# Kernel tuning notes

Measured on AMD Instinct MI355X. Metric: run time of the kernel, lower is better.

## Reference

```python
import jax, jax.numpy as jnp
import numpy as np

# --- configuration constants (from OpticalDotProductConfiguration) ---
INPUT_BITS = 8
ADC_BITS = 8
DAC_VMIN, DAC_VMAX = 0.0, 1.0
ADC_VMAX = 1.0
OPT_GAIN = 10.0
AWG_XTALK = 0.01
MZM_VMIN, MZM_VMAX = 0.0, 1.0
MZM_LOSS = 10.0 ** (-0.5 / 10.0)   # loss_dB_to_linear(0.5)
YB_LOSS = 10.0 ** (-0.3 / 10.0)
MRR_LOSS = 10.0 ** (-0.5 / 10.0)
MRR_XTALK = 0.01
PD_RESP = 1.0
PD_DARK = 1e-12
PD_R = 50.0
PD_HZ = 10.0 * 1e9
PD_T = 300.0
TIA_GAIN = 100.0
K_B = 1.380649e-23
Q_E = 1.602176634e-19

B, N = 4096, 8192


def conv_same(x, kernel):
    # x: [B, N], kernel: [K]; torch F.conv1d = cross-correlation, same as lax conv
    out = jax.lax.conv_general_dilated(
        x[:, None, :], kernel[None, None, :], (1,), 'SAME')
    return out[:, 0, :]


def setup_inputs() -> dict:
    key = jax.random.key(0)
    ks = jax.random.split(key, 6)
    return {
        'x': jax.random.normal(ks[0], (B, N), dtype=jnp.float32),
        'weights': jax.random.normal(ks[1], (N,), dtype=jnp.float32),
        'noise_tp': jax.random.normal(ks[2], (B,), dtype=jnp.float32),
        'noise_sp': jax.random.normal(ks[3], (B,), dtype=jnp.float32),
        'noise_tn': jax.random.normal(ks[4], (B,), dtype=jnp.float32),
        'noise_sn': jax.random.normal(ks[5], (B,), dtype=jnp.float32),
    }


def reference(x, weights, noise_tp, noise_sp, noise_tn, noise_sn):
    dt = x.dtype
    # software_implemented_transformation
    wnorm = jnp.max(jnp.abs(weights))
    wnorm = jnp.where(wnorm <= 1e-9, jnp.asarray(1.0, dt), wnorm)
    wt = weights / wnorm
    w_abs = jnp.abs(wt)            # weight DAC is identity for weights
    w_pos = wt >= 0                # [N] bool

    t_pos = x > 0                  # [B, N]
    ax = jnp.abs(x)
    inorm = jnp.max(ax, axis=1)
    inorm = jnp.where(inorm <= 1e-9, jnp.asarray(1.0, dt), inorm)[:, None]
    maxq_in = 2 ** INPUT_BITS - 1
    q = jnp.round(ax / inorm * maxq_in)

    # input DAC
    d = jnp.round(jnp.clip(q, 0.0, maxq_in)) / maxq_in
    d = DAC_VMIN + (DAC_VMAX - DAC_VMIN) * d

    # laser: gain + AWG crosstalk conv
    lk = jnp.array([AWG_XTALK / 4, AWG_XTALK, 1.0, AWG_XTALK, AWG_XTALK / 4], dtype=dt)
    l = conv_same(d * OPT_GAIN, lk)

    # MZM
    m = l * w_abs / (MZM_VMAX - MZM_VMIN) * (YB_LOSS * MZM_LOSS)

    # MRR: masked split, crosstalk conv, loss, reduce over N
    pm = jnp.logical_not(jnp.logical_xor(w_pos[None, :], t_pos)).astype(dt)
    mk = jnp.array([MRR_XTALK / 4, MRR_XTALK, 1.0, MRR_XTALK, MRR_XTALK / 4], dtype=dt)
    pos_sum = jnp.sum(conv_same(m * pm, mk) * MRR_LOSS, axis=1)        # [B]
    neg_sum = jnp.sum(conv_same(m * (1.0 - pm), mk) * MRR_LOSS, axis=1)

    # photodiode with injected noise
    thermal_c = 4.0 * K_B * PD_T * PD_HZ / PD_R
    shot_c = 2.0 * Q_E * PD_HZ

    def pd(t, nth, nsh):
        t = t * PD_RESP + PD_DARK
        t = t + nth * thermal_c
        return t * (1.0 + nsh * shot_c)

    cur = pd(pos_sum, noise_tp, noise_sp) - pd(neg_sum, noise_tn, noise_sn)

    # TIA
    v = jnp.abs(cur * TIA_GAIN)
    sign = (cur >= 0).astype(dt) * 2.0 - 1.0

    # ADC
    sf = (2 ** ADC_BITS - 1) / ADC_VMAX
    va = jnp.round(jnp.clip(v, 0.0, ADC_VMAX) * sf) / sf
    out = va * sign

    scale = wnorm / (2.0 ** (ADC_BITS - INPUT_BITS))
    scale = scale / (OPT_GAIN * TIA_GAIN * MRR_LOSS * YB_LOSS * MZM_LOSS)
    scale = scale / ((PD_RESP + PD_RESP) / 2.0)
    out = out * (scale * inorm[:, 0])
    return out
```

## Files before the change

### kernel.cpp

```cpp
#include <hip/hip_runtime.h>
#include <math.h>

#define NCOL 8192
#define BT   512
#define EPT  16

#define MZM_LOSS_D 0.8912509381337456
#define YB_LOSS_D  0.9332543007969910
#define MRR_LOSS_D 0.8912509381337456

__global__ __launch_bounds__(BT, 6)
void odp_main(const float* __restrict__ x, const float* __restrict__ w,
              const float* __restrict__ ntp, const float* __restrict__ nsp,
              const float* __restrict__ ntn, const float* __restrict__ nsn,
              float* __restrict__ out)
{
    __shared__ float  redX[8];
    __shared__ float  redW[8];
    __shared__ float  redT[8];
    __shared__ double redD[8];
    __shared__ double corrd[4];

    const int t    = threadIdx.x;
    const int lane = t & 63;
    const int wid  = t >> 6;
    const int b    = blockIdx.x;

    const float v_ntp = ntp[b], v_nsp = nsp[b], v_ntn = ntn[b], v_nsn = nsn[b];

    const float*  __restrict__ xrow = x + (size_t)b * NCOL;
    const float4* __restrict__ xr4  = (const float4*)xrow;
    const float4* __restrict__ w4   = (const float4*)w;

    float xf[EPT];
    const int hL = (t > 0)      ? (t * EPT - 2)   : 0;
    const int hR = (t < BT - 1) ? (t * EPT + EPT) : (NCOL - 2);
    const float2 hxL = *(const float2*)(xrow + hL);
    const float2 hxR = *(const float2*)(xrow + hR);

    float mx = 0.f;
#pragma unroll
    for (int j = 0; j < 4; ++j) {
        const float4 xv = xr4[t * 4 + j];
        xf[4*j+0]=xv.x; xf[4*j+1]=xv.y; xf[4*j+2]=xv.z; xf[4*j+3]=xv.w;
        mx = fmaxf(mx, fmaxf(fmaxf(fabsf(xv.x), fabsf(xv.y)),
                             fmaxf(fabsf(xv.z), fabsf(xv.w))));
    }
#pragma unroll
    for (int off = 32; off; off >>= 1)
        mx = fmaxf(mx, __shfl_down(mx, off));
    if (lane == 0) redX[wid] = mx;
    __syncthreads();

    float inorm = redX[0];
#pragma unroll
    for (int i = 1; i < 8; ++i) inorm = fmaxf(inorm, redX[i]);
    inorm = (inorm <= 1e-9f) ? 1.f : inorm;

    const double inv_d = 1.0 / (double)inorm;
    const float  y     = (float)inv_d;

    float wf[EPT];
    float mw = 0.f;
#pragma unroll
    for (int j = 0; j < 4; ++j) {
        const float4 wv = w4[t * 4 + j];
        wf[4*j+0]=wv.x; wf[4*j+1]=wv.y; wf[4*j+2]=wv.z; wf[4*j+3]=wv.w;
        mw = fmaxf(mw, fmaxf(fmaxf(fabsf(wv.x), fabsf(wv.y)),
                             fmaxf(fabsf(wv.z), fabsf(wv.w))));
    }

    float Q[EPT + 4];
#pragma unroll
    for (int c = 0; c < EPT; ++c) {
        const float a  = fabsf(xf[c]);
        const float q0 = a * y;
        const float r  = fmaf(-inorm, q0, a);
        Q[c + 2] = rintf(fmaf(r, y, q0) * 255.f);
    }
    {
        const float aL0 = fabsf(hxL.x), aL1 = fabsf(hxL.y);
        const float aR0 = fabsf(hxR.x), aR1 = fabsf(hxR.y);
        float q0, r;
        q0 = aL0 * y; r = fmaf(-inorm, q0, aL0); Q[0]  = rintf(fmaf(r, y, q0) * 255.f);
        q0 = aL1 * y; r = fmaf(-inorm, q0, aL1); Q[1]  = rintf(fmaf(r, y, q0) * 255.f);
        q0 = aR0 * y; r = fmaf(-inorm, q0, aR0); Q[18] = rintf(fmaf(r, y, q0) * 255.f);
        q0 = aR1 * y; r = fmaf(-inorm, q0, aR1); Q[19] = rintf(fmaf(r, y, q0) * 255.f);
        if (t == 0)      { Q[0]  = 0.f; Q[1]  = 0.f; }
        if (t == BT - 1) { Q[18] = 0.f; Q[19] = 0.f; }
    }

    float Dv[4] = {0.f,0.f,0.f,0.f}, Tv[4] = {0.f,0.f,0.f,0.f};
    double cD = 0.0, cT = 0.0;
    const double DE0 = -((double)0.01f + (double)0.0025f);
    const double DE1 = -((double)0.0025f);

#pragma unroll
    for (int c = 0; c < EPT; ++c) {
        const float s1 = Q[c + 1] + Q[c + 3];
        const float s2 = Q[c]     + Q[c + 4];
        float conv = fmaf(0.01f, s1, Q[c + 2]);
        conv = fmaf(0.0025f, s2, conv);
        const float sel = (xf[c] > 0.f) ? wf[c] : -wf[c];
        Dv[c & 3] = fmaf(conv, sel,        Dv[c & 3]);
        Tv[c & 3] = fmaf(conv, fabsf(sel), Tv[c & 3]);
    }
    if (t == 0) {
#pragma unroll
        for (int c = 0; c < 2; ++c) {
            const float s1 = Q[c + 1] + Q[c + 3];
            const float s2 = Q[c]     + Q[c + 4];
            float conv = fmaf(0.01f, s1, Q[c + 2]);
            conv = fmaf(0.0025f, s2, conv);
            const float sel = (xf[c] > 0.f) ? wf[c] : -wf[c];
            const double de = (c == 0) ? DE0 : DE1;
            cD += de * (double)(conv * sel);
            cT += de * (double)(conv * fabsf(sel));
        }
    }
    if (t == BT - 1) {
#pragma unroll
        for (int c = EPT - 2; c < EPT; ++c) {
            const float s1 = Q[c + 1] + Q[c + 3];
            const float s2 = Q[c]     + Q[c + 4];
            float conv = fmaf(0.01f, s1, Q[c + 2]);
            conv = fmaf(0.0025f, s2, conv);
            const float sel = (xf[c] > 0.f) ? wf[c] : -wf[c];
            const double de = (c == EPT - 1) ? DE0 : DE1;
            cD += de * (double)(conv * sel);
            cT += de * (double)(conv * fabsf(sel));
        }
    }

    double accD = ((double)Dv[0] + (double)Dv[1]) + ((double)Dv[2] + (double)Dv[3]);
    float  accT = (Tv[0] + Tv[1]) + (Tv[2] + Tv[3]);

#pragma unroll
    for (int off = 32; off; off >>= 1) {
        accD += __shfl_down(accD, off);
        accT += __shfl_down(accT, off);
        mw    = fmaxf(mw, __shfl_down(mw, off));
    }
    if (lane == 0)   { redD[wid] = accD; redT[wid] = accT; redW[wid] = mw; }
    if (t == 0)      { corrd[0] = cD; corrd[1] = cT; }
    if (t == BT - 1) { corrd[2] = cD; corrd[3] = cT; }
    __syncthreads();

    if (t == 0) {
        double D = 0.0, T = 0.0;
        float wnorm = redW[0];
#pragma unroll
        for (int i = 0; i < 8; ++i) {
            D += redD[i]; T += (double)redT[i];
            wnorm = fmaxf(wnorm, redW[i]);
        }
        wnorm = (wnorm <= 1e-9f) ? 1.f : wnorm;

        const double E_MID = 1.0 + 2.0 * (double)0.01f + 2.0 * (double)0.0025f;
        D = D * E_MID + (corrd[0] + corrd[2]);
        T = T * E_MID + (corrd[1] + corrd[3]);

        const double Kd = (10.0 / 255.0) * (YB_LOSS_D * MZM_LOSS_D) / (double)wnorm;
        const double ps = (T + D) * 0.5 * Kd * MRR_LOSS_D;
        const double ns = (T - D) * 0.5 * Kd * MRR_LOSS_D;

        const float thermal_f = 3.3135576e-12f;
        const float shot_f    = 3.204353268e-9f;

        double tp_ = ps + 1e-12 + (double)(v_ntp * thermal_f);
        tp_ *= (double)(1.0f + v_nsp * shot_f);
        double tn_ = ns + 1e-12 + (double)(v_ntn * thermal_f);
        tn_ *= (double)(1.0f + v_nsn * shot_f);

        const double cur = tp_ - tn_;
        double v = fabs(cur * 100.0);
        v = fmin(v, 1.0);
        const double va  = rint(v * 255.0) * (1.0 / 255.0);
        const double sgn = (cur >= 0.0) ? 1.0 : -1.0;
        const double scale = (double)wnorm /
            (10.0 * 100.0 * MRR_LOSS_D * YB_LOSS_D * MZM_LOSS_D);
        out[b] = (float)(va * sgn * scale * (double)inorm);
    }
}

extern "C" void kernel_launch(void* const* d_in, const int* in_sizes, int n_in,
                              void* d_out, int out_size, void* d_ws, size_t ws_size,
                              hipStream_t stream) {
    const float* x   = (const float*)d_in[0];
    const float* w   = (const float*)d_in[1];
    const float* ntp = (const float*)d_in[2];
    const float* nsp = (const float*)d_in[3];
    const float* ntn = (const float*)d_in[4];
    const float* nsn = (const float*)d_in[5];
    float* out = (float*)d_out;
    odp_main<<<dim3(out_size), dim3(BT), 0, stream>>>(x, w, ntp, nsp, ntn, nsn, out);
}
```

Baseline: 32.67 us.

## Process eight rows per block with double-buffered async global-to-LDS loads

```diff
diff --git a/kernel.cpp b/kernel.cpp
--- a/kernel.cpp
+++ b/kernel.cpp
@@ -4,62 +4,51 @@
 #define NCOL 8192
 #define BT   512
 #define EPT  16
+#define ROWS 8
+#define NF4  2048
 
 #define MZM_LOSS_D 0.8912509381337456
 #define YB_LOSS_D  0.9332543007969910
 #define MRR_LOSS_D 0.8912509381337456
 
-__global__ __launch_bounds__(BT, 6)
+typedef __attribute__((address_space(3))) void       lds_void_t;
+typedef const __attribute__((address_space(1))) void g_void_t;
+
+static __device__ __forceinline__ void lds_barrier() {
+    asm volatile("s_waitcnt lgkmcnt(0)" ::: "memory");
+    __builtin_amdgcn_s_barrier();
+}
+
+static __device__ __forceinline__ int swz(int g) { return g ^ ((g >> 3) & 7); }
+
+#define QF(dst, a_) do {                                   \
+    const float a__  = (a_);                               \
+    const float q0__ = a__ * y;                            \
+    const float r__  = fmaf(-inorm, q0__, a__);            \
+    (dst) = rintf(fmaf(r__, y, q0__) * 255.f);             \
+} while (0)
+
+__global__ __launch_bounds__(BT, 4)
 void odp_main(const float* __restrict__ x, const float* __restrict__ w,
               const float* __restrict__ ntp, const float* __restrict__ nsp,
               const float* __restrict__ ntn, const float* __restrict__ nsn,
               float* __restrict__ out)
 {
-    __shared__ float  redX[8];
-    __shared__ float  redW[8];
-    __shared__ float  redT[8];
+    __shared__ float4 xs[2][NF4];
+    __shared__ float  redX[8], redW[8], redT[8];
     __shared__ double redD[8];
     __shared__ double corrd[4];
 
     const int t    = threadIdx.x;
     const int lane = t & 63;
     const int wid  = t >> 6;
-    const int b    = blockIdx.x;
-
-    const float v_ntp = ntp[b], v_nsp = nsp[b], v_ntn = ntn[b], v_nsn = nsn[b];
-
-    const float*  __restrict__ xrow = x + (size_t)b * NCOL;
-    const float4* __restrict__ xr4  = (const float4*)xrow;
-    const float4* __restrict__ w4   = (const float4*)w;
-
-    float xf[EPT];
-    const int hL = (t > 0)      ? (t * EPT - 2)   : 0;
-    const int hR = (t < BT - 1) ? (t * EPT + EPT) : (NCOL - 2);
-    const float2 hxL = *(const float2*)(xrow + hL);
-    const float2 hxR = *(const float2*)(xrow + hR);
-
-    float mx = 0.f;
-#pragma unroll
-    for (int j = 0; j < 4; ++j) {
-        const float4 xv = xr4[t * 4 + j];
-        xf[4*j+0]=xv.x; xf[4*j+1]=xv.y; xf[4*j+2]=xv.z; xf[4*j+3]=xv.w;
-        mx = fmaxf(mx, fmaxf(fmaxf(fabsf(xv.x), fabsf(xv.y)),
-                             fmaxf(fabsf(xv.z), fabsf(xv.w))));
-    }
-#pragma unroll
-    for (int off = 32; off; off >>= 1)
-        mx = fmaxf(mx, __shfl_down(mx, off));
-    if (lane == 0) redX[wid] = mx;
-    __syncthreads();
-
-    float inorm = redX[0];
-#pragma unroll
-    for (int i = 1; i < 8; ++i) inorm = fmaxf(inorm, redX[i]);
-    inorm = (inorm <= 1e-9f) ? 1.f : inorm;
-
-    const double inv_d = 1.0 / (double)inorm;
-    const float  y     = (float)inv_d;
-
+    const int r0   = blockIdx.x * ROWS;
+
+    const double DE0 = -((double)0.01f + (double)0.0025f);
+    const double DE1 = -((double)0.0025f);
+    const double E_MID = 1.0 + 2.0 * (double)0.01f + 2.0 * (double)0.0025f;
+
+    const float4* __restrict__ w4 = (const float4*)w;
     float wf[EPT];
     float mw = 0.f;
 #pragma unroll
@@ -70,117 +59,168 @@
                              fmaxf(fabsf(wv.z), fabsf(wv.w))));
     }
 
-    float Q[EPT + 4];
-#pragma unroll
-    for (int c = 0; c < EPT; ++c) {
-        const float a  = fabsf(xf[c]);
-        const float q0 = a * y;
-        const float r  = fmaf(-inorm, q0, a);
-        Q[c + 2] = rintf(fmaf(r, y, q0) * 255.f);
-    }
-    {
-        const float aL0 = fabsf(hxL.x), aL1 = fabsf(hxL.y);
-        const float aR0 = fabsf(hxR.x), aR1 = fabsf(hxR.y);
-        float q0, r;
-        q0 = aL0 * y; r = fmaf(-inorm, q0, aL0); Q[0]  = rintf(fmaf(r, y, q0) * 255.f);
-        q0 = aL1 * y; r = fmaf(-inorm, q0, aL1); Q[1]  = rintf(fmaf(r, y, q0) * 255.f);
-        q0 = aR0 * y; r = fmaf(-inorm, q0, aR0); Q[18] = rintf(fmaf(r, y, q0) * 255.f);
-        q0 = aR1 * y; r = fmaf(-inorm, q0, aR1); Q[19] = rintf(fmaf(r, y, q0) * 255.f);
+#define STAGE(BUF, ROW) do {                                                  \
+    const float* xr_ = x + (size_t)(ROW) * NCOL;                              \
+    _Pragma("unroll")                                                         \
+    for (int k = 0; k < 4; ++k) {                                             \
+        const int phys_ = ((wid * 4 + k) << 6) | lane;                        \
+        __builtin_amdgcn_global_load_lds(                                     \
+            (g_void_t*)(xr_ + 4 * swz(phys_)),                                \
+            (lds_void_t*)&xs[BUF][(wid * 4 + k) << 6], 16, 0, 0);             \
+    }                                                                         \
+} while (0)
+
+    STAGE(0, r0);
+
+    int wi[4];
+#pragma unroll
+    for (int k = 0; k < 4; ++k) wi[k] = swz(4 * t + k);
+    const int hiL = swz((t > 0)      ? (4 * t - 1) : 0);
+    const int hiR = swz((t < BT - 1) ? (4 * t + 4) : (NF4 - 1));
+
+    float wnorm = 1.f;
+    float ov[ROWS];
+
+#pragma unroll
+    for (int r = 0; r < ROWS; ++r) {
+        const int buf = r & 1;
+        if (r < ROWS - 1) {
+            STAGE(buf ^ 1, r0 + r + 1);
+            asm volatile("s_waitcnt vmcnt(4)" ::: "memory");
+        } else {
+            asm volatile("s_waitcnt vmcnt(0)" ::: "memory");
+        }
+
+        float xf[EPT];
+#pragma unroll
+        for (int k = 0; k < 4; ++k) {
+            const float4 v = xs[buf][wi[k]];
+            xf[4*k+0]=v.x; xf[4*k+1]=v.y; xf[4*k+2]=v.z; xf[4*k+3]=v.w;
+        }
+        float mx = 0.f;
+#pragma unroll
+        for (int c = 0; c < EPT; ++c) mx = fmaxf(mx, fabsf(xf[c]));
+#pragma unroll
+        for (int off = 32; off; off >>= 1)
+            mx = fmaxf(mx, __shfl_down(mx, off));
+        if (lane == 0) redX[wid] = mx;
+        lds_barrier();
+
+        float inorm = redX[0];
+#pragma unroll
+        for (int i = 1; i < 8; ++i) inorm = fmaxf(inorm, redX[i]);
+        inorm = (inorm <= 1e-9f) ? 1.f : inorm;
+        const double inv_d = 1.0 / (double)inorm;
+        const float  y     = (float)inv_d;
+
+        const float4 hv1 = xs[buf][hiL];
+        const float4 hv2 = xs[buf][hiR];
+
+        float Q[EPT + 4];
+#pragma unroll
+        for (int c = 0; c < EPT; ++c) QF(Q[c + 2], fabsf(xf[c]));
+        QF(Q[0],  fabsf(hv1.z)); QF(Q[1],  fabsf(hv1.w));
+        QF(Q[18], fabsf(hv2.x)); QF(Q[19], fabsf(hv2.y));
         if (t == 0)      { Q[0]  = 0.f; Q[1]  = 0.f; }
         if (t == BT - 1) { Q[18] = 0.f; Q[19] = 0.f; }
-    }
-
-    float Dv[4] = {0.f,0.f,0.f,0.f}, Tv[4] = {0.f,0.f,0.f,0.f};
-    double cD = 0.0, cT = 0.0;
-    const double DE0 = -((double)0.01f + (double)0.0025f);
-    const double DE1 = -((double)0.0025f);
-
-#pragma unroll
-    for (int c = 0; c < EPT; ++c) {
-        const float s1 = Q[c + 1] + Q[c + 3];
-        const float s2 = Q[c]     + Q[c + 4];
-        float conv = fmaf(0.01f, s1, Q[c + 2]);
-        conv = fmaf(0.0025f, s2, conv);
-        const float sel = (xf[c] > 0.f) ? wf[c] : -wf[c];
-        Dv[c & 3] = fmaf(conv, sel,        Dv[c & 3]);
-        Tv[c & 3] = fmaf(conv, fabsf(sel), Tv[c & 3]);
-    }
-    if (t == 0) {
-#pragma unroll
-        for (int c = 0; c < 2; ++c) {
+
+        float Dv[4] = {0.f,0.f,0.f,0.f}, Tv[4] = {0.f,0.f,0.f,0.f};
+        double cD = 0.0, cT = 0.0;
+#pragma unroll
+        for (int c = 0; c < EPT; ++c) {
             const float s1 = Q[c + 1] + Q[c + 3];
             const float s2 = Q[c]     + Q[c + 4];
-            float conv = fmaf(0.01f, s1, Q[c + 2]);
-            conv = fmaf(0.0025f, s2, conv);
+            float cv = fmaf(0.01f, s1, Q[c + 2]);
+            cv = fmaf(0.0025f, s2, cv);
             const float sel = (xf[c] > 0.f) ? wf[c] : -wf[c];
-            const double de = (c == 0) ? DE0 : DE1;
-            cD += de * (double)(conv * sel);
-            cT += de * (double)(conv * fabsf(sel));
+            Dv[c & 3] = fmaf(cv, sel,        Dv[c & 3]);
+            Tv[c & 3] = fmaf(cv, fabsf(sel), Tv[c & 3]);
+        }
+        if (t == 0) {
+#pragma unroll
+            for (int c = 0; c < 2; ++c) {
+                const float s1 = Q[c + 1] + Q[c + 3];
+                const float s2 = Q[c]     + Q[c + 4];
+                float cv = fmaf(0.01f, s1, Q[c + 2]);
+                cv = fmaf(0.0025f, s2, cv);
+                const float sel = (xf[c] > 0.f) ? wf[c] : -wf[c];
+                const double de = (c == 0) ? DE0 : DE1;
+                cD += de * (double)(cv * sel);
+                cT += de * (double)(cv * fabsf(sel));
+            }
+        }
+        if (t == BT - 1) {
+#pragma unroll
+            for (int c = EPT - 2; c < EPT; ++c) {
+                const float s1 = Q[c + 1] + Q[c + 3];
+                const float s2 = Q[c]     + Q[c + 4];
+                float cv = fmaf(0.01f, s1, Q[c + 2]);
+                cv = fmaf(0.0025f, s2, cv);
+                const float sel = (xf[c] > 0.f) ? wf[c] : -wf[c];
+                const double de = (c == EPT - 1) ? DE0 : DE1;
+                cD += de * (double)(cv * sel);
+                cT += de * (double)(cv * fabsf(sel));
+            }
+        }
+
+        double accD = ((double)Dv[0] + (double)Dv[1]) + ((double)Dv[2] + (double)Dv[3]);
+        float  accT = (Tv[0] + Tv[1]) + (Tv[2] + Tv[3]);
+        float  mww  = mw;
+#pragma unroll
+        for (int off = 32; off; off >>= 1) {
+            accD += __shfl_down(accD, off);
+            accT += __shfl_down(accT, off);
+            mww   = fmaxf(mww, __shfl_down(mww, off));
+        }
+        if (lane == 0)   { redD[wid] = accD; redT[wid] = accT; redW[wid] = mww; }
+        if (t == 0)      { corrd[0] = cD; corrd[1] = cT; }
+        if (t == BT - 1) { corrd[2] = cD; corrd[3] = cT; }
+        lds_barrier();
+
+        if (t == 0) {
+            double D = 0.0, T = 0.0;
+            float wn = redW[0];
+#pragma unroll
+            for (int i = 0; i < 8; ++i) {
+                D += redD[i]; T += (double)redT[i];
+                wn = fmaxf(wn, redW[i]);
+            }
+            if (r == 0) wnorm = (wn <= 1e-9f) ? 1.f : wn;
+
+            D = D * E_MID + (corrd[0] + corrd[2]);
+            T = T * E_MID + (corrd[1] + corrd[3]);
+
+            const double Kd = (10.0 / 255.0) * (YB_LOSS_D * MZM_LOSS_D) / (double)wnorm;
+            const double ps = (T + D) * 0.5 * Kd * MRR_LOSS_D;
+            const double ns = (T - D) * 0.5 * Kd * MRR_LOSS_D;
+
+            const float thermal_f = 3.3135576e-12f;
+            const float shot_f    = 3.204353268e-9f;
+            const int   row_      = r0 + r;
+
+            double tp_ = ps + 1e-12 + (double)(ntp[row_] * thermal_f);
+            tp_ *= (double)(1.0f + nsp[row_] * shot_f);
+            double tn_ = ns + 1e-12 + (double)(ntn[row_] * thermal_f);
+            tn_ *= (double)(1.0f + nsn[row_] * shot_f);
+
+            const double cur = tp_ - tn_;
+            double v = fabs(cur * 100.0);
+            v = fmin(v, 1.0);
+            const double va  = rint(v * 255.0) * (1.0 / 255.0);
+            const double sgn = (cur >= 0.0) ? 1.0 : -1.0;
+            const double scale = (double)wnorm /
+                (10.0 * 100.0 * MRR_LOSS_D * YB_LOSS_D * MZM_LOSS_D);
+            ov[r] = (float)(va * sgn * scale * (double)inorm);
         }
     }
-    if (t == BT - 1) {
-#pragma unroll
-        for (int c = EPT - 2; c < EPT; ++c) {
-            const float s1 = Q[c + 1] + Q[c + 3];
-            const float s2 = Q[c]     + Q[c + 4];
-            float conv = fmaf(0.01f, s1, Q[c + 2]);
-            conv = fmaf(0.0025f, s2, conv);
-            const float sel = (xf[c] > 0.f) ? wf[c] : -wf[c];
-            const double de = (c == EPT - 1) ? DE0 : DE1;
-            cD += de * (double)(conv * sel);
-            cT += de * (double)(conv * fabsf(sel));
-        }
+
+    if (t == 0) {
+        float4 o0 = make_float4(ov[0], ov[1], ov[2], ov[3]);
+        float4 o1 = make_float4(ov[4], ov[5], ov[6], ov[7]);
+        *(float4*)(out + r0)     = o0;
+        *(float4*)(out + r0 + 4) = o1;
     }
-
-    double accD = ((double)Dv[0] + (double)Dv[1]) + ((double)Dv[2] + (double)Dv[3]);
-    float  accT = (Tv[0] + Tv[1]) + (Tv[2] + Tv[3]);
-
-#pragma unroll
-    for (int off = 32; off; off >>= 1) {
-        accD += __shfl_down(accD, off);
-        accT += __shfl_down(accT, off);
-        mw    = fmaxf(mw, __shfl_down(mw, off));
-    }
-    if (lane == 0)   { redD[wid] = accD; redT[wid] = accT; redW[wid] = mw; }
-    if (t == 0)      { corrd[0] = cD; corrd[1] = cT; }
-    if (t == BT - 1) { corrd[2] = cD; corrd[3] = cT; }
-    __syncthreads();
-
-    if (t == 0) {
-        double D = 0.0, T = 0.0;
-        float wnorm = redW[0];
-#pragma unroll
-        for (int i = 0; i < 8; ++i) {
-            D += redD[i]; T += (double)redT[i];
-            wnorm = fmaxf(wnorm, redW[i]);
-        }
-        wnorm = (wnorm <= 1e-9f) ? 1.f : wnorm;
-
-        const double E_MID = 1.0 + 2.0 * (double)0.01f + 2.0 * (double)0.0025f;
-        D = D * E_MID + (corrd[0] + corrd[2]);
-        T = T * E_MID + (corrd[1] + corrd[3]);
-
-        const double Kd = (10.0 / 255.0) * (YB_LOSS_D * MZM_LOSS_D) / (double)wnorm;
-        const double ps = (T + D) * 0.5 * Kd * MRR_LOSS_D;
-        const double ns = (T - D) * 0.5 * Kd * MRR_LOSS_D;
-
-        const float thermal_f = 3.3135576e-12f;
-        const float shot_f    = 3.204353268e-9f;
-
-        double tp_ = ps + 1e-12 + (double)(v_ntp * thermal_f);
-        tp_ *= (double)(1.0f + v_nsp * shot_f);
-        double tn_ = ns + 1e-12 + (double)(v_ntn * thermal_f);
-        tn_ *= (double)(1.0f + v_nsn * shot_f);
-
-        const double cur = tp_ - tn_;
-        double v = fabs(cur * 100.0);
-        v = fmin(v, 1.0);
-        const double va  = rint(v * 255.0) * (1.0 / 255.0);
-        const double sgn = (cur >= 0.0) ? 1.0 : -1.0;
-        const double scale = (double)wnorm /
-            (10.0 * 100.0 * MRR_LOSS_D * YB_LOSS_D * MZM_LOSS_D);
-        out[b] = (float)(va * sgn * scale * (double)inorm);
-    }
+#undef STAGE
 }
 
 extern "C" void kernel_launch(void* const* d_in, const int* in_sizes, int n_in,
@@ -193,5 +233,6 @@
     const float* ntn = (const float*)d_in[4];
     const float* nsn = (const float*)d_in[5];
     float* out = (float*)d_out;
-    odp_main<<<dim3(out_size), dim3(BT), 0, stream>>>(x, w, ntp, nsp, ntn, nsn, out);
+    const int nblocks = out_size / ROWS;
+    odp_main<<<dim3(nblocks), dim3(BT), 0, stream>>>(x, w, ntp, nsp, ntn, nsn, out);
 }
```

Result: slower. 36.58 us, median of 4 (+12.0%).
